# Optimization experiments

Hardware: AMD Instinct MI355X
Metric: run time of the kernel (lower is better)

## Reference

```python
import jax, jax.numpy as jnp
import numpy as np

SIDE = 32
RADIUS = 6.0
N_CHANNEL = 64
KEY_SIZE = 32


def _dist_mask(side, radius):
    # dists[x1, y1, x2, y2] = euclidean distance; flatten (x1,y1) -> N
    xs = jnp.arange(side, dtype=jnp.float32)
    dx = xs[:, None, None, None] - xs[None, None, :, None]  # X1 - X2
    dy = xs[None, :, None, None] - xs[None, None, None, :]  # Y1 - Y2
    d = jnp.sqrt(dx * dx + dy * dy)                          # (s,s,s,s)
    d = d.reshape(side * side, side, side)                   # (N, H, W)
    return jnp.where(d > radius, -jnp.inf, 0.0)[None]        # (1, N, H, W)


def setup_inputs() -> dict:
    key = jax.random.key(0)
    ks = jax.random.split(key, 8)
    B = 16
    x = jax.random.normal(ks[0], (B, N_CHANNEL, SIDE, SIDE), dtype=jnp.float32)
    s_c = 1.0 / np.sqrt(N_CHANNEL)
    s_k = 1.0 / np.sqrt(KEY_SIZE)
    Wq = jax.random.normal(ks[1], (KEY_SIZE, N_CHANNEL), dtype=jnp.float32) * s_c
    Wk = jax.random.normal(ks[2], (KEY_SIZE, N_CHANNEL), dtype=jnp.float32) * s_c
    Wv = jax.random.normal(ks[3], (KEY_SIZE, N_CHANNEL), dtype=jnp.float32) * s_c
    Wq_xy = jax.random.normal(ks[4], (2, N_CHANNEL), dtype=jnp.float32) * s_c
    Wk_xy = jax.random.normal(ks[5], (2, N_CHANNEL), dtype=jnp.float32) * s_c
    Wout = jax.random.normal(ks[6], (N_CHANNEL, KEY_SIZE), dtype=jnp.float32) * s_k
    return {"x": x, "Wq": Wq, "Wk": Wk, "Wv": Wv,
            "Wq_xy": Wq_xy, "Wk_xy": Wk_xy, "Wout": Wout}


def reference(x, Wq, Wk, Wv, Wq_xy, Wk_xy, Wout):
    B, C, H, W = x.shape
    N = H * W
    mask = _dist_mask(H, RADIUS)  # (1, N, H, W)

    # 1x1 convs == channel contractions
    q = jnp.einsum('kc,bchw->bkhw', Wq, x)                 # (B,K,H,W) queries
    k = jnp.einsum('kc,bchw->bkhw', Wk, x).reshape(B, -1, N)   # (B,K,N) keys (flattened)
    v = jnp.einsum('kc,bchw->bkhw', Wv, x).reshape(B, -1, N)   # (B,K,N) values
    q_xy = jnp.einsum('kc,bchw->bkhw', Wq_xy, x)           # (B,2,H,W)
    k_xy = jnp.einsum('kc,bchw->bkhw', Wk_xy, x).reshape(B, 2, N)

    # scores[b,n,h,w]: key n vs query (h,w)
    scores = jnp.einsum('bkn,bkhw->bnhw', k, q)
    scores_xy = jnp.einsum('bkn,bkhw->bnhw', k_xy, q_xy)
    attn = jax.nn.softmax(scores_xy + mask + scores, axis=1)   # over N keys

    out = jnp.einsum('bnhw,bkn->bkhw', attn, v)            # (B,K,H,W)
    return jnp.einsum('ck,bkhw->bchw', Wout, out)          # (B,C,H,W)
```

## Files before the change

### kernel.cpp

```cpp
#include <hip/hip_runtime.h>
#include <math.h>

typedef short bf16x8 __attribute__((ext_vector_type(8)));
typedef float f32x4 __attribute__((ext_vector_type(4)));
typedef unsigned short u16;
typedef unsigned int u32;

#define WS_QT  0
#define WS_KT  1048576
#define WS_VW  2097152
#define WS_QXY 3153920
#define WS_KXY 3284992
#define VWS    1032

__device__ __forceinline__ u32 f2bf(float f) {
    u32 u = __float_as_uint(f);
    u += 0x7fffu + ((u >> 16) & 1u);
    return u >> 16;
}
__device__ __forceinline__ u32 pk2(float a, float b) {
    return f2bf(a) | (f2bf(b) << 16);
}

union U4H { uint4 u; bf16x8 h; };

__global__ __launch_bounds__(64) void proj_kernel(
    const float* __restrict__ x,
    const float* __restrict__ Wq, const float* __restrict__ Wk,
    const float* __restrict__ Wv, const float* __restrict__ Wqxy,
    const float* __restrict__ Wkxy, char* __restrict__ wsb)
{
    u16* QT = (u16*)(wsb + WS_QT);
    u16* KT = (u16*)(wsb + WS_KT);
    u16* VW = (u16*)(wsb + WS_VW);
    float* QXY = (float*)(wsb + WS_QXY);
    float* KXY = (float*)(wsb + WS_KXY);

    int l = threadIdx.x;
    int g = l >> 4, l15 = l & 15;
    int bid = blockIdx.x;
    int xcd = bid & 7, j = bid >> 3;
    int b = (xcd << 1) + (j >> 6);
    int n0 = (j & 63) << 4;

    bf16x8 ah[2], al[2];
    #pragma unroll
    for (int ks = 0; ks < 2; ks++) {
        float av[8];
        #pragma unroll
        for (int i = 0; i < 8; i++)
            av[i] = x[(((b << 6) + (ks << 5) + (g << 3) + i) << 10) + n0 + l15];
        #pragma unroll
        for (int i = 0; i < 8; i++) {
            u32 hb = f2bf(av[i]);
            float rr = av[i] - __uint_as_float(hb << 16);
            ah[ks][i] = (short)hb;
            al[ks][i] = (short)f2bf(rr);
        }
    }

    #pragma unroll
    for (int jt = 0; jt < 7; jt++) {
        f32x4 acc = {0.f, 0.f, 0.f, 0.f};
        #pragma unroll
        for (int ks = 0; ks < 2; ks++) {
            float wv[8];
            #pragma unroll
            for (int i = 0; i < 8; i++) wv[i] = 0.f;
            if (jt < 6) {
                const float* wbase = (jt < 2) ? Wq : (jt < 4) ? Wk : Wv;
                const float* wr = wbase + ((((jt & 1) << 4) + l15) << 6)
                                        + (ks << 5) + (g << 3);
                float4 wa = *(const float4*)wr, wb = *(const float4*)(wr + 4);
                wv[0] = wa.x; wv[1] = wa.y; wv[2] = wa.z; wv[3] = wa.w;
                wv[4] = wb.x; wv[5] = wb.y; wv[6] = wb.z; wv[7] = wb.w;
            } else if (l15 < 4) {
                const float* wr = ((l15 < 2) ? (Wqxy + (l15 << 6))
                                             : (Wkxy + ((l15 - 2) << 6)))
                                  + (ks << 5) + (g << 3);
                float4 wa = *(const float4*)wr, wb = *(const float4*)(wr + 4);
                wv[0] = wa.x; wv[1] = wa.y; wv[2] = wa.z; wv[3] = wa.w;
                wv[4] = wb.x; wv[5] = wb.y; wv[6] = wb.z; wv[7] = wb.w;
            }
            bf16x8 wh, wl;
            #pragma unroll
            for (int i = 0; i < 8; i++) {
                u32 hb = f2bf(wv[i]);
                float rr = wv[i] - __uint_as_float(hb << 16);
                wh[i] = (short)hb;
                wl[i] = (short)f2bf(rr);
            }
            acc = __builtin_amdgcn_mfma_f32_16x16x32_bf16(ah[ks], wh, acc, 0, 0, 0);
            acc = __builtin_amdgcn_mfma_f32_16x16x32_bf16(al[ks], wh, acc, 0, 0, 0);
            acc = __builtin_amdgcn_mfma_f32_16x16x32_bf16(ah[ks], wl, acc, 0, 0, 0);
        }
        if (jt < 2) {
            #pragma unroll
            for (int r = 0; r < 4; r++)
                QT[(((b << 10) + n0 + (g << 2) + r) << 5) + (jt << 4) + l15]
                    = (u16)f2bf(acc[r]);
        } else if (jt < 4) {
            #pragma unroll
            for (int r = 0; r < 4; r++)
                KT[(((b << 10) + n0 + (g << 2) + r) << 5) + ((jt - 2) << 4) + l15]
                    = (u16)f2bf(acc[r]);
        } else if (jt < 6) {
            int kd = ((jt - 4) << 4) + l15;
            uint2 d = make_uint2(pk2(acc[0], acc[1]), pk2(acc[2], acc[3]));
            *(uint2*)&VW[((b << 5) + kd) * VWS + n0 + (g << 2)] = d;
        } else {
            if (l15 < 2) {
                #pragma unroll
                for (int r = 0; r < 4; r++)
                    QXY[(((b << 10) + n0 + (g << 2) + r) << 1) + l15] = acc[r];
            } else if (l15 < 4) {
                #pragma unroll
                for (int r = 0; r < 4; r++)
                    KXY[(((b << 10) + n0 + (g << 2) + r) << 1) + (l15 - 2)] = acc[r];
            }
        }
    }

    if ((j & 63) == 63 && l < 32)
        *(uint4*)&VW[((b << 5) + l) * VWS + 1024] = make_uint4(0, 0, 0, 0);
}

__global__ __launch_bounds__(256, 3) void attn_kernel(
    const char* __restrict__ wsb, const float* __restrict__ Wout,
    float* __restrict__ out)
{
    const u16* QT = (const u16*)(wsb + WS_QT);
    const u16* KT = (const u16*)(wsb + WS_KT);
    const u16* VW = (const u16*)(wsb + WS_VW);
    const float* QXY = (const float*)(wsb + WS_QXY);
    const float* KXY = (const float*)(wsb + WS_KXY);

    __shared__ __align__(16) u16 kfr[20 * 64 * 8];
    __shared__ __align__(16) u16 vfr[10 * 128 * 8];
    __shared__ __align__(16) u32 kxyb[320 * 2];
    __shared__ __align__(16) u16 wfr[4 * 64 * 8];
    __shared__ __align__(16) u16 o_l[4 * 8 * 32];

    int tid = threadIdx.x, bid = blockIdx.x;
    int xcd = bid & 7, j = bid >> 3;
    int b = (xcd << 1) + (j >> 5);
    int t5 = j & 31;
    int qy0 = (t5 >> 3) << 3, qx0 = (t5 & 7) << 2;
    int ry0 = qy0 - 6, rx0 = qx0 - 6;

    #pragma unroll
    for (int i = 0; i < 5; i++) {
        int c = tid + (i << 8);
        int t = c >> 6, g2 = (c >> 4) & 3, sc = c & 15;
        int n2 = (ry0 + t) * 32 + rx0 + sc;
        n2 = max(0, min(1023, n2));
        uint4 d = *(const uint4*)(KT + (((b << 10) + n2) << 5) + (g2 << 3));
        *(uint4*)&kfr[c << 3] = d;
    }
    #pragma unroll
    for (int i = 0; i < 10; i++) {
        int d = tid + (i << 8);
        int p = d & 1, kd = (d >> 1) & 31, g2 = (d >> 6) & 3, kk = d >> 8;
        int ky = ry0 + (kk << 1) + p;
        int n = ky * 32 + rx0 + (g2 << 2);
        if ((u32)ky > 31u) n = 0;
        const u32* s = (const u32*)(VW + ((b << 5) + kd) * VWS + n);
        *(uint2*)&vfr[d << 2] = make_uint2(s[0], s[1]);
    }
    for (int i = tid; i < 320; i += 256) {
        int n2 = (ry0 + (i >> 4)) * 32 + rx0 + (i & 15);
        n2 = max(0, min(1023, n2));
        float2 f = *(const float2*)(KXY + (((b << 10) + n2) << 1));
        u32 h0 = f2bf(f.x), h1 = f2bf(f.y);
        float r0 = f.x - __uint_as_float(h0 << 16);
        float r1 = f.y - __uint_as_float(h1 << 16);
        kxyb[(i << 1)]     = h0 | (h1 << 16);
        kxyb[(i << 1) + 1] = f2bf(r0) | (f2bf(r1) << 16);
    }
    {
        int nt = tid >> 6, l = tid & 63;
        int cc = (nt << 4) + (l & 15);
        const float* wsrc = Wout + (cc << 5) + ((l >> 4) << 3);
        uint4 dw;
        dw.x = pk2(wsrc[0], wsrc[1]); dw.y = pk2(wsrc[2], wsrc[3]);
        dw.z = pk2(wsrc[4], wsrc[5]); dw.w = pk2(wsrc[6], wsrc[7]);
        *(uint4*)&wfr[tid << 3] = dw;
    }

    int w = tid >> 6, ll = tid & 63;
    int lq = ll & 15, g = ll >> 4;
    int qloc = lq & 7;
    int qrow = (w << 1) + (qloc >> 2), qcol = qloc & 3;
    int nq = (qy0 + qrow) * 32 + qx0 + qcol;
    uint4 bqu = *(const uint4*)(QT + (((b << 10) + nq) << 5) + (g << 3));
    float2 qv = *(const float2*)(QXY + (((b << 10) + nq) << 1));
    u32 qh0 = f2bf(qv.x), qh1 = f2bf(qv.y);
    float qr0 = qv.x - __uint_as_float(qh0 << 16);
    float qr1 = qv.y - __uint_as_float(qh1 << 16);
    u32 qhp = qh0 | (qh1 << 16);
    u32 qlp = f2bf(qr0) | (f2bf(qr1) << 16);
    uint4 bxyu = make_uint4(g == 0 ? qhp : 0, g == 0 ? qlp : 0,
                            g == 0 ? qhp : 0, 0);

    __syncthreads();

    f32x4 acc[20];
    #pragma unroll
    for (int t = 0; t < 20; t++) {
        uint2 kp = *(const uint2*)&kxyb[((t << 4) + lq) << 1];
        U4H axy; axy.u = make_uint4(g == 0 ? kp.x : 0, g == 0 ? kp.x : 0,
                                    g == 0 ? kp.y : 0, 0);
        U4H bxy; bxy.u = bxyu;
        f32x4 z = {0.f, 0.f, 0.f, 0.f};
        f32x4 a0 = __builtin_amdgcn_mfma_f32_16x16x32_bf16(axy.h, bxy.h, z, 0, 0, 0);
        U4H ak; ak.u = *(const uint4*)&kfr[((t << 6) + (g << 4) + lq) << 3];
        U4H bq; bq.u = bqu;
        acc[t] = __builtin_amdgcn_mfma_f32_16x16x32_bf16(ak.h, bq.h, a0, 0, 0, 0);
    }

    int dx2a[4], kxa[4];
    #pragma unroll
    for (int r = 0; r < 4; r++) {
        int sc = (g << 2) + r;
        int kx = rx0 + sc;
        kxa[r] = (kx >= 0) && (kx < 32);
        int dx = sc - 6 - qcol;
        dx2a[r] = dx * dx;
    }
    float m = -1e30f;
    #pragma unroll
    for (int t = 0; t < 20; t++) {
        int ky = ry0 + t;
        bool kyok = (ky >= 0) && (ky < 32);
        int dy = t - 6 - qrow, dy2 = dy * dy;
        #pragma unroll
        for (int r = 0; r < 4; r++) {
            bool ok = kyok && kxa[r] && (dy2 + dx2a[r] <= 36);
            acc[t][r] = ok ? acc[t][r] : -1e4f;
            m = fmaxf(m, acc[t][r]);
        }
    }
    m = fmaxf(m, __shfl_xor(m, 16, 64));
    m = fmaxf(m, __shfl_xor(m, 32, 64));

    float sum = 0.f;
    #pragma unroll
    for (int t = 0; t < 20; t++) {
        #pragma unroll
        for (int r = 0; r < 4; r++) {
            float e = __expf(acc[t][r] - m);
            acc[t][r] = e;
            sum += e;
        }
    }
    sum += __shfl_xor(sum, 16, 64);
    sum += __shfl_xor(sum, 32, 64);

    float rinv = 1.f / sum;
    #pragma unroll
    for (int t = 0; t < 20; t++) {
        #pragma unroll
        for (int r = 0; r < 4; r++) acc[t][r] *= rinv;
    }

    f32x4 o0 = {0.f, 0.f, 0.f, 0.f}, o1 = {0.f, 0.f, 0.f, 0.f};
    #pragma unroll
    for (int kk = 0; kk < 10; kk++) {
        U4H pa;
        pa.u = make_uint4(pk2(acc[2 * kk][0],     acc[2 * kk][1]),
                          pk2(acc[2 * kk][2],     acc[2 * kk][3]),
                          pk2(acc[2 * kk + 1][0], acc[2 * kk + 1][1]),
                          pk2(acc[2 * kk + 1][2], acc[2 * kk + 1][3]));
        U4H v0; v0.u = *(const uint4*)&vfr[((kk << 7) + (g << 5) + lq) << 3];
        U4H v1; v1.u = *(const uint4*)&vfr[((kk << 7) + (g << 5) + lq + 16) << 3];
        o0 = __builtin_amdgcn_mfma_f32_16x16x32_bf16(pa.h, v0.h, o0, 0, 0, 0);
        o1 = __builtin_amdgcn_mfma_f32_16x16x32_bf16(pa.h, v1.h, o1, 0, 0, 0);
    }

    if (g < 2) {
        #pragma unroll
        for (int r = 0; r < 4; r++) {
            int q = (g << 2) + r;
            o_l[(w << 8) + (q << 5) + lq]      = (u16)f2bf(o0[r]);
            o_l[(w << 8) + (q << 5) + lq + 16] = (u16)f2bf(o1[r]);
        }
    }
    __syncthreads();

    U4H aO; aO.u = *(const uint4*)&o_l[(w << 8) + (qloc << 5) + (g << 3)];
    int nqb = (qy0 + (w << 1) + g) * 32 + qx0;
    #pragma unroll
    for (int nt2 = 0; nt2 < 4; nt2++) {
        U4H bw; bw.u = *(const uint4*)&wfr[((nt2 << 6) + ll) << 3];
        f32x4 z = {0.f, 0.f, 0.f, 0.f};
        f32x4 y = __builtin_amdgcn_mfma_f32_16x16x32_bf16(aO.h, bw.h, z, 0, 0, 0);
        if (g < 2) {
            int cc = (nt2 << 4) + lq;
            #pragma unroll
            for (int r = 0; r < 4; r++)
                out[(((b << 6) + cc) << 10) + nqb + r] = y[r];
        }
    }
}

extern "C" void kernel_launch(void* const* d_in, const int* in_sizes, int n_in,
                              void* d_out, int out_size, void* d_ws, size_t ws_size,
                              hipStream_t stream) {
    const float* x    = (const float*)d_in[0];
    const float* Wq   = (const float*)d_in[1];
    const float* Wk   = (const float*)d_in[2];
    const float* Wv   = (const float*)d_in[3];
    const float* Wqxy = (const float*)d_in[4];
    const float* Wkxy = (const float*)d_in[5];
    const float* Wout = (const float*)d_in[6];
    float* out = (float*)d_out;
    char* wsb  = (char*)d_ws;

    proj_kernel<<<1024, 64, 0, stream>>>(x, Wq, Wk, Wv, Wqxy, Wkxy, wsb);
    attn_kernel<<<512, 256, 0, stream>>>(wsb, Wout, out);
}
```

Before: 19.84 us.

## Enlarge attention query tile to 16x4 so waves share a taller key halo

Each attention block now covers 16 query rows by 4 columns instead of 8x4. The four waves each take 16 query positions (4 rows) and a 16-row slice of a shared 28-row key/value halo in LDS. This lowers the halo overhead per query, halves the grid to 256 blocks, and lets every MFMA lane do useful work in the output projection. In exchange the staged LDS is larger and reused via aliasing, an extra barrier is added, occupancy drops to 1 block per SM, and the grid may be too small to fill all CUs.

```diff
diff --git a/kernel.cpp b/kernel.cpp
--- a/kernel.cpp
+++ b/kernel.cpp
@@ -125,7 +125,7 @@
         *(uint4*)&VW[((b << 5) + l) * VWS + 1024] = make_uint4(0, 0, 0, 0);
 }
 
-__global__ __launch_bounds__(256, 3) void attn_kernel(
+__global__ __launch_bounds__(256, 1) void attn_kernel(
     const char* __restrict__ wsb, const float* __restrict__ Wout,
     float* __restrict__ out)
 {
@@ -135,21 +135,22 @@
     const float* QXY = (const float*)(wsb + WS_QXY);
     const float* KXY = (const float*)(wsb + WS_KXY);
 
-    __shared__ __align__(16) u16 kfr[20 * 64 * 8];
-    __shared__ __align__(16) u16 vfr[10 * 128 * 8];
-    __shared__ __align__(16) u32 kxyb[320 * 2];
-    __shared__ __align__(16) u16 wfr[4 * 64 * 8];
-    __shared__ __align__(16) u16 o_l[4 * 8 * 32];
+    __shared__ __align__(16) u16 smem[32512];
+    u16* kfr = smem;
+    u16* vfr = smem + 14336;
+    u32* kxyb = (u32*)(smem + 28672);
+    u16* wfr = smem + 30464;
+    u16* o_l = smem;
 
     int tid = threadIdx.x, bid = blockIdx.x;
     int xcd = bid & 7, j = bid >> 3;
-    int b = (xcd << 1) + (j >> 5);
-    int t5 = j & 31;
-    int qy0 = (t5 >> 3) << 3, qx0 = (t5 & 7) << 2;
+    int b = (xcd << 1) + (j >> 4);
+    int t4 = j & 15;
+    int qy0 = (t4 >> 3) << 4, qx0 = (t4 & 7) << 2;
     int ry0 = qy0 - 6, rx0 = qx0 - 6;
 
     #pragma unroll
-    for (int i = 0; i < 5; i++) {
+    for (int i = 0; i < 7; i++) {
         int c = tid + (i << 8);
         int t = c >> 6, g2 = (c >> 4) & 3, sc = c & 15;
         int n2 = (ry0 + t) * 32 + rx0 + sc;
@@ -158,16 +159,16 @@
         *(uint4*)&kfr[c << 3] = d;
     }
     #pragma unroll
-    for (int i = 0; i < 10; i++) {
+    for (int i = 0; i < 14; i++) {
         int d = tid + (i << 8);
-        int p = d & 1, kd = (d >> 1) & 31, g2 = (d >> 6) & 3, kk = d >> 8;
-        int ky = ry0 + (kk << 1) + p;
+        int p = d & 1, kd = (d >> 1) & 31, g2 = (d >> 6) & 3, m = d >> 8;
+        int ky = ry0 + (m << 1) + p;
         int n = ky * 32 + rx0 + (g2 << 2);
         if ((u32)ky > 31u) n = 0;
         const u32* s = (const u32*)(VW + ((b << 5) + kd) * VWS + n);
         *(uint2*)&vfr[d << 2] = make_uint2(s[0], s[1]);
     }
-    for (int i = tid; i < 320; i += 256) {
+    for (int i = tid; i < 448; i += 256) {
         int n2 = (ry0 + (i >> 4)) * 32 + rx0 + (i & 15);
         n2 = max(0, min(1023, n2));
         float2 f = *(const float2*)(KXY + (((b << 10) + n2) << 1));
@@ -189,9 +190,8 @@
 
     int w = tid >> 6, ll = tid & 63;
     int lq = ll & 15, g = ll >> 4;
-    int qloc = lq & 7;
-    int qrow = (w << 1) + (qloc >> 2), qcol = qloc & 3;
-    int nq = (qy0 + qrow) * 32 + qx0 + qcol;
+    int qrl = lq >> 2, qcol = lq & 3;
+    int nq = (qy0 + (w << 2) + qrl) * 32 + qx0 + qcol;
     uint4 bqu = *(const uint4*)(QT + (((b << 10) + nq) << 5) + (g << 3));
     float2 qv = *(const float2*)(QXY + (((b << 10) + nq) << 1));
     u32 qh0 = f2bf(qv.x), qh1 = f2bf(qv.y);
@@ -204,16 +204,17 @@
 
     __syncthreads();
 
-    f32x4 acc[20];
-    #pragma unroll
-    for (int t = 0; t < 20; t++) {
-        uint2 kp = *(const uint2*)&kxyb[((t << 4) + lq) << 1];
+    f32x4 acc[16];
+    #pragma unroll
+    for (int t = 0; t < 16; t++) {
+        int rr = (w << 2) + t;
+        uint2 kp = *(const uint2*)&kxyb[((rr << 4) + lq) << 1];
         U4H axy; axy.u = make_uint4(g == 0 ? kp.x : 0, g == 0 ? kp.x : 0,
                                     g == 0 ? kp.y : 0, 0);
         U4H bxy; bxy.u = bxyu;
         f32x4 z = {0.f, 0.f, 0.f, 0.f};
         f32x4 a0 = __builtin_amdgcn_mfma_f32_16x16x32_bf16(axy.h, bxy.h, z, 0, 0, 0);
-        U4H ak; ak.u = *(const uint4*)&kfr[((t << 6) + (g << 4) + lq) << 3];
+        U4H ak; ak.u = *(const uint4*)&kfr[((rr << 6) + (g << 4) + lq) << 3];
         U4H bq; bq.u = bqu;
         acc[t] = __builtin_amdgcn_mfma_f32_16x16x32_bf16(ak.h, bq.h, a0, 0, 0, 0);
     }
@@ -229,10 +230,10 @@
     }
     float m = -1e30f;
     #pragma unroll
-    for (int t = 0; t < 20; t++) {
-        int ky = ry0 + t;
+    for (int t = 0; t < 16; t++) {
+        int ky = ry0 + (w << 2) + t;
         bool kyok = (ky >= 0) && (ky < 32);
-        int dy = t - 6 - qrow, dy2 = dy * dy;
+        int dy = t - 6 - qrl, dy2 = dy * dy;
         #pragma unroll
         for (int r = 0; r < 4; r++) {
             bool ok = kyok && kxa[r] && (dy2 + dx2a[r] <= 36);
@@ -245,7 +246,7 @@
 
     float sum = 0.f;
     #pragma unroll
-    for (int t = 0; t < 20; t++) {
+    for (int t = 0; t < 16; t++) {
         #pragma unroll
         for (int r = 0; r < 4; r++) {
             float e = __expf(acc[t][r] - m);
@@ -258,48 +259,46 @@
 
     float rinv = 1.f / sum;
     #pragma unroll
-    for (int t = 0; t < 20; t++) {
+    for (int t = 0; t < 16; t++) {
         #pragma unroll
         for (int r = 0; r < 4; r++) acc[t][r] *= rinv;
     }
 
     f32x4 o0 = {0.f, 0.f, 0.f, 0.f}, o1 = {0.f, 0.f, 0.f, 0.f};
     #pragma unroll
-    for (int kk = 0; kk < 10; kk++) {
+    for (int kk = 0; kk < 8; kk++) {
+        int m2 = (w << 1) + kk;
         U4H pa;
         pa.u = make_uint4(pk2(acc[2 * kk][0],     acc[2 * kk][1]),
                           pk2(acc[2 * kk][2],     acc[2 * kk][3]),
                           pk2(acc[2 * kk + 1][0], acc[2 * kk + 1][1]),
                           pk2(acc[2 * kk + 1][2], acc[2 * kk + 1][3]));
-        U4H v0; v0.u = *(const uint4*)&vfr[((kk << 7) + (g << 5) + lq) << 3];
-        U4H v1; v1.u = *(const uint4*)&vfr[((kk << 7) + (g << 5) + lq + 16) << 3];
+        U4H v0; v0.u = *(const uint4*)&vfr[((m2 << 7) + (g << 5) + lq) << 3];
+        U4H v1; v1.u = *(const uint4*)&vfr[((m2 << 7) + (g << 5) + lq + 16) << 3];
         o0 = __builtin_amdgcn_mfma_f32_16x16x32_bf16(pa.h, v0.h, o0, 0, 0, 0);
         o1 = __builtin_amdgcn_mfma_f32_16x16x32_bf16(pa.h, v1.h, o1, 0, 0, 0);
     }
 
-    if (g < 2) {
-        #pragma unroll
-        for (int r = 0; r < 4; r++) {
-            int q = (g << 2) + r;
-            o_l[(w << 8) + (q << 5) + lq]      = (u16)f2bf(o0[r]);
-            o_l[(w << 8) + (q << 5) + lq + 16] = (u16)f2bf(o1[r]);
-        }
-    }
     __syncthreads();
-
-    U4H aO; aO.u = *(const uint4*)&o_l[(w << 8) + (qloc << 5) + (g << 3)];
-    int nqb = (qy0 + (w << 1) + g) * 32 + qx0;
+    #pragma unroll
+    for (int r = 0; r < 4; r++) {
+        int q = (g << 2) + r;
+        o_l[(w << 9) + (q << 5) + lq]      = (u16)f2bf(o0[r]);
+        o_l[(w << 9) + (q << 5) + lq + 16] = (u16)f2bf(o1[r]);
+    }
+    __syncthreads();
+
+    U4H aO; aO.u = *(const uint4*)&o_l[(w << 9) + (lq << 5) + (g << 3)];
+    int nqb = (qy0 + (w << 2) + g) * 32 + qx0;
     #pragma unroll
     for (int nt2 = 0; nt2 < 4; nt2++) {
         U4H bw; bw.u = *(const uint4*)&wfr[((nt2 << 6) + ll) << 3];
         f32x4 z = {0.f, 0.f, 0.f, 0.f};
         f32x4 y = __builtin_amdgcn_mfma_f32_16x16x32_bf16(aO.h, bw.h, z, 0, 0, 0);
-        if (g < 2) {
-            int cc = (nt2 << 4) + lq;
-            #pragma unroll
-            for (int r = 0; r < 4; r++)
-                out[(((b << 6) + cc) << 10) + nqb + r] = y[r];
-        }
+        int cc = (nt2 << 4) + lq;
+        #pragma unroll
+        for (int r = 0; r < 4; r++)
+            out[(((b << 6) + cc) << 10) + nqb + r] = y[r];
     }
 }
 
@@ -317,5 +316,5 @@
     char* wsb  = (char*)d_ws;
 
     proj_kernel<<<1024, 64, 0, stream>>>(x, Wq, Wk, Wv, Wqxy, Wkxy, wsb);
-    attn_kernel<<<512, 256, 0, stream>>>(wsb, Wout, out);
-}
+    attn_kernel<<<256, 256, 0, stream>>>(wsb, Wout, out);
+}
```

After: 18.41 us, median of 2. 7.2% less time.
